# Performance work log

Hardware: AMD Instinct MI355X
Metric: run time of the kernel (lower is better)

The kernel has to match this reference:

```python
import jax, jax.numpy as jnp
import numpy as np

B, N1, N2, E = 128, 128, 384, 1024
N = N1 + N2
D_IN, D_FC = 64, 128
NUM_HEADS = 8.0  # args.num_att_heads
THETA = 1.0      # args.al_scale


def setup_inputs() -> dict:
    key = jax.random.key(0)
    ks = jax.random.split(key, 14)
    c_hs = jax.random.normal(ks[0], (B, N, D_IN), jnp.float32)
    attention = jax.random.uniform(ks[1], (B, N1, N2), jnp.float32)
    coords = jax.random.normal(ks[2], (B, N, 3), jnp.float32)
    upd_coords = coords + 0.1 * jax.random.normal(ks[3], (B, N, 3), jnp.float32)
    c_valid = jnp.ones((B, N), jnp.float32)
    nm = (jax.random.uniform(ks[4], (B, N1)) < 0.7).astype(jnp.float32)
    mapping = (jax.random.uniform(ks[5], (B, N, N)) < 0.05).astype(jnp.float32)
    samelb = jnp.maximum(mapping, (jax.random.uniform(ks[6], (B, N, N)) < 0.1).astype(jnp.float32))
    edge_index = jax.random.randint(ks[7], (B, E, 2), 0, N1, jnp.int32)
    W0 = jax.random.normal(ks[8], (D_IN, D_FC), jnp.float32) * 0.05
    b0 = jnp.zeros((D_FC,), jnp.float32)
    W1 = jax.random.normal(ks[9], (D_FC, D_FC), jnp.float32) * 0.05
    b1 = jnp.zeros((D_FC,), jnp.float32)
    W2 = jax.random.normal(ks[10], (D_FC, D_FC), jnp.float32) * 0.05
    b2 = jnp.zeros((D_FC,), jnp.float32)
    W3 = jax.random.normal(ks[11], (D_FC, 1), jnp.float32) * 0.05
    b3 = jnp.zeros((1,), jnp.float32)
    return dict(c_hs=c_hs, attention=attention, coords=coords, upd_coords=upd_coords,
                c_valid=c_valid, nm=nm, mapping=mapping, samelb=samelb,
                edge_index=edge_index, W0=W0, b0=b0, W1=W1, b1=b1, W2=W2, b2=b2, W3=W3, b3=b3)


def _kabsch(P, Q, m):
    # P, Q: [N1, 3], m: [N1] 0/1 non-modified mask
    Pm = P.mean(0)
    Qm = Q.mean(0)
    h = (P - Pm).T @ (Q - Qm) / NUM_HEADS  # [3,3]
    u, s, vt = jnp.linalg.svd(h)
    d = jnp.sign(jnp.linalg.det(h))
    corr = jnp.diag(jnp.concatenate([jnp.ones((2,), h.dtype), d[None].astype(h.dtype)]))
    r = u @ corr @ vt
    trans = Qm - r @ Pm
    Pp = P @ r.T + trans
    mk = (m > 0.5).astype(P.dtype)[:, None]
    cnt = jnp.maximum(mk.sum() * 3.0, 1.0)
    new_rmsd = (mk * (Pp - Q) ** 2).sum() / cnt        # mse over selected rows
    cen = ((Pp.mean(0) - Qm) ** 2).mean()              # centroid mse
    return new_rmsd, cen


def reference(c_hs, attention, coords, upd_coords, c_valid, nm, mapping, samelb,
              edge_index, W0, b0, W1, b1, W2, b2, W3, b3):
    # --- segment-sum pooling (sum_var_parts) + divide by n1, then FC head ---
    pooled = (c_hs * c_valid[..., None]).sum(axis=1) / float(N1)   # [B, D_IN]
    h = jax.nn.relu(pooled @ W0 + b0)
    h = jax.nn.relu(h @ W1 + b1)
    h = jax.nn.relu(h @ W2 + b2)
    scores = jax.nn.sigmoid(h @ W3 + b3).reshape(-1)               # [B]

    # --- cal_atten_batch + F.normalize(dim=1) ---
    atten = jnp.zeros((B, N, N), c_hs.dtype)
    atten = atten.at[:, :N1, N1:].set(attention)
    atten = atten.at[:, N1:, :N1].set(jnp.swapaxes(attention, 1, 2))
    nrm = jnp.sqrt((atten ** 2).sum(axis=1, keepdims=True))
    atten = atten / jnp.maximum(nrm, 1e-12)

    # --- cal_attn_loss ---
    top = jnp.where(mapping == 1.0, jnp.exp(-(atten * mapping)), 0.0).sum(axis=(1, 2))
    topabot = jnp.where(samelb == 1.0, jnp.exp(-(atten * samelb)), 0.0).sum(axis=(1, 2))
    attn_loss = (top / (topabot - top + 1.0)).sum() * THETA / float(B)

    # --- cal_rmsd_loss: straight-through one-hot mapping + Kabsch/SVD ---
    PP = upd_coords[:, :N1]   # subgraph updated coords
    QQ = coords[:, N1:]       # target graph original coords
    oh = jax.nn.one_hot(jnp.argmax(attention, axis=-1), N2, dtype=attention.dtype)
    st = oh + attention - jax.lax.stop_gradient(attention)         # straight-through
    Qsel = jnp.einsum('bij,bjd->bid', st, QQ)                      # [B, N1, 3]
    new_rmsd, cen = jax.vmap(_kabsch)(PP, Qsel, nm)
    rmsd_loss = new_rmsd.mean()
    centroid_loss = cen.mean()

    # --- cal_pairdst_loss over subgraph edges ---
    sub_c = coords[:, :N1]
    sub_u = upd_coords[:, :N1]
    bidx = jnp.arange(B)[:, None]
    d0 = jnp.sqrt(((sub_c[bidx, edge_index[..., 0]] - sub_c[bidx, edge_index[..., 1]]) ** 2).sum(-1) + 1e-12)
    d1 = jnp.sqrt(((sub_u[bidx, edge_index[..., 0]] - sub_u[bidx, edge_index[..., 1]]) ** 2).sum(-1) + 1e-12)
    pairdst_loss = jnp.abs((d1 - d0).sum(axis=-1)).mean()

    return scores, attn_loss, rmsd_loss, pairdst_loss, centroid_loss
```

## Files before the change

### kernel.cpp

```cpp
#include <hip/hip_runtime.h>
#include <math.h>

#define B_   128
#define N1_  128
#define N2_  384
#define N_   512
#define E_   1024
#define DIN  64
#define DFC  128

#define ACC_TOP  0
#define ACC_BOT  128
#define POOL_OFF 256
#define RNI_OFF  (POOL_OFF + B_*DIN)
#define BI_OFF   (RNI_OFF + B_*N1_)
#define CNI_OFF  (BI_OFF + B_*N1_)

typedef float f4v __attribute__((ext_vector_type(4)));
__device__ __forceinline__ float4 ntl4(const float4* p) {
    f4v v = __builtin_nontemporal_load((const f4v*)p);
    float4 r; r.x = v.x; r.y = v.y; r.z = v.z; r.w = v.w;
    return r;
}

__global__ void k_init(float* ws, float* out) {
    int idx = blockIdx.x * 256 + threadIdx.x;
    if (idx < 256 + B_ * DIN) ws[idx] = 0.f;
    if (idx < B_ * N2_) ws[CNI_OFF + idx] = 0.f;
    if (idx < 4) out[128 + idx] = 0.f;
}

__global__ void k_front(const float* __restrict__ c_hs, const float* __restrict__ c_valid,
                        const float* __restrict__ att, float* __restrict__ ws) {
    __shared__ float4 sred4[256];
    int b = blockIdx.x, y = blockIdx.y, t = threadIdx.x;
    if (y < 8) {
        int chunk = y * 64;
        int d4 = t & 15, rl = t >> 4;
        const float4* X4 = (const float4*)(c_hs + (size_t)b * N_ * DIN);
        const float* V = c_valid + (size_t)b * N_;
        float4 acc = {0.f, 0.f, 0.f, 0.f};
        #pragma unroll
        for (int r = chunk + rl; r < chunk + 64; r += 16) {
            float4 x = ntl4(&X4[r * 16 + d4]);
            float v = V[r];
            acc.x += x.x * v; acc.y += x.y * v; acc.z += x.z * v; acc.w += x.w * v;
        }
        sred4[t] = acc; __syncthreads();
        for (int off = 128; off >= 16; off >>= 1) {
            if (t < off) {
                float4 o = sred4[t + off];
                sred4[t].x += o.x; sred4[t].y += o.y; sred4[t].z += o.z; sred4[t].w += o.w;
            }
            __syncthreads();
        }
        if (t < 16) {
            float4 s = sred4[t];
            float* p = ws + POOL_OFF + b * DIN + t * 4;
            atomicAdd(&p[0], s.x); atomicAdd(&p[1], s.y);
            atomicAdd(&p[2], s.z); atomicAdd(&p[3], s.w);
        }
        return;
    }
    float* colacc = (float*)sred4;
    for (int c = t; c < N2_; c += 256) colacc[c] = 0.f;
    __syncthreads();
    int wv = t >> 6, ln = t & 63;
    int r = (y - 8) * 4 + wv;
    const float* row = att + ((size_t)b * N1_ + r) * N2_;
    float vv[6];
    float ssq = 0.f, best = -1e30f; int bidx = 0;
    #pragma unroll
    for (int q = 0; q < 6; ++q) {
        float v = row[ln + 64 * q];
        vv[q] = v;
        ssq += v * v;
        if (v > best) { best = v; bidx = ln + 64 * q; }
    }
    #pragma unroll
    for (int q = 0; q < 6; ++q) atomicAdd(&colacc[ln + 64 * q], vv[q] * vv[q]);
    for (int off = 32; off > 0; off >>= 1) {
        ssq += __shfl_xor(ssq, off, 64);
        float ov = __shfl_xor(best, off, 64);
        int oi = __shfl_xor(bidx, off, 64);
        if (ov > best || (ov == best && oi < bidx)) { best = ov; bidx = oi; }
    }
    if (ln == 0) {
        ws[RNI_OFF + b * N1_ + r] = 1.f / fmaxf(sqrtf(ssq), 1e-12f);
        ((int*)ws)[BI_OFF + b * N1_ + r] = bidx;
    }
    __syncthreads();
    for (int c = t; c < N2_; c += 256)
        atomicAdd(&ws[CNI_OFF + b * N2_ + c], colacc[c]);
}

__global__ void k_fin(float* __restrict__ ws) {
    int b = blockIdx.x, t = threadIdx.x;
    float v = ws[CNI_OFF + b * N2_ + t];
    ws[CNI_OFF + b * N2_ + t] = 1.f / fmaxf(sqrtf(v), 1e-12f);
}

#define EWS 132
__global__ __launch_bounds__(256, 4)
void k_scan(const float* __restrict__ att, const float* __restrict__ mapping,
            const float* __restrict__ samelb, float* __restrict__ ws) {
    __shared__ float ew[8 * EWS];
    __shared__ float rt[4], rb[4];
    int d = blockIdx.x;
    int xcd = d & 7, kk = d >> 3;
    int b = xcd * 16 + (kk >> 6);
    int tile = kk & 63;
    int t = threadIdx.x;
    float top = 0.f, bot = 0.f;
    int r = t >> 5, c4 = t & 31;
    if (tile < 16) {
        int i0 = tile * 8;
        const float4* m4 = (const float4*)(mapping + ((size_t)b * N_ + i0) * N_);
        const float4* s4 = (const float4*)(samelb + ((size_t)b * N_ + i0) * N_);
        const float4* a4 = (const float4*)(att + ((size_t)b * N1_ + i0) * N2_);
        const float4* cn4 = (const float4*)(ws + CNI_OFF + (size_t)b * N2_);
        float4 md = ntl4(&m4[r * 128 + c4]);
        float4 sd = ntl4(&s4[r * 128 + c4]);
        float4 av[3], mv[3], sv[3], cn[3];
        #pragma unroll
        for (int k = 0; k < 3; ++k) {
            int c = c4 + 32 * k;
            av[k] = a4[r * 96 + c];
            mv[k] = ntl4(&m4[r * 128 + 32 + c]);
            sv[k] = ntl4(&s4[r * 128 + 32 + c]);
            cn[k] = cn4[c];
        }
        top = md.x + md.y + md.z + md.w;
        bot = sd.x + sd.y + sd.z + sd.w;
        #pragma unroll
        for (int k = 0; k < 3; ++k) {
            float e0 = __expf(-av[k].x * cn[k].x);
            float e1 = __expf(-av[k].y * cn[k].y);
            float e2 = __expf(-av[k].z * cn[k].z);
            float e3 = __expf(-av[k].w * cn[k].w);
            top += mv[k].x * e0 + mv[k].y * e1 + mv[k].z * e2 + mv[k].w * e3;
            bot += sv[k].x * e0 + sv[k].y * e1 + sv[k].z * e2 + sv[k].w * e3;
        }
    } else {
        int tb = tile - 16;
        int cr0 = tb * 8;
        const float4* a4 = (const float4*)(att + (size_t)b * N1_ * N2_);
        {
            int j = t >> 1, q = t & 1;
            float4 a = a4[j * 96 + tb * 2 + q];
            float rv = ws[RNI_OFF + b * N1_ + j];
            ew[(4 * q + 0) * EWS + j] = __expf(-a.x * rv);
            ew[(4 * q + 1) * EWS + j] = __expf(-a.y * rv);
            ew[(4 * q + 2) * EWS + j] = __expf(-a.z * rv);
            ew[(4 * q + 3) * EWS + j] = __expf(-a.w * rv);
        }
        const float4* m4 = (const float4*)(mapping + ((size_t)b * N_ + N1_ + cr0) * N_);
        const float4* s4 = (const float4*)(samelb + ((size_t)b * N_ + N1_ + cr0) * N_);
        float4 mL = ntl4(&m4[r * 128 + c4]);
        float4 sL = ntl4(&s4[r * 128 + c4]);
        float4 mR[3], sR[3];
        #pragma unroll
        for (int k = 0; k < 3; ++k) {
            int c = c4 + 32 * k;
            mR[k] = ntl4(&m4[r * 128 + 32 + c]);
            sR[k] = ntl4(&s4[r * 128 + 32 + c]);
        }
        __syncthreads();
        float4 w = *(const float4*)&ew[r * EWS + c4 * 4];
        top = mL.x * w.x + mL.y * w.y + mL.z * w.z + mL.w * w.w;
        bot = sL.x * w.x + sL.y * w.y + sL.z * w.z + sL.w * w.w;
        #pragma unroll
        for (int k = 0; k < 3; ++k) {
            top += mR[k].x + mR[k].y + mR[k].z + mR[k].w;
            bot += sR[k].x + sR[k].y + sR[k].z + sR[k].w;
        }
    }
    for (int off = 32; off > 0; off >>= 1) {
        top += __shfl_down(top, off, 64);
        bot += __shfl_down(bot, off, 64);
    }
    int wv = t >> 6, ln = t & 63;
    if (ln == 0) { rt[wv] = top; rb[wv] = bot; }
    __syncthreads();
    if (t == 0) {
        atomicAdd(&ws[ACC_TOP + b], rt[0] + rt[1] + rt[2] + rt[3]);
        atomicAdd(&ws[ACC_BOT + b], rb[0] + rb[1] + rb[2] + rb[3]);
    }
}

__device__ inline float bred(float* s2, float v, int t) {
    for (int off = 32; off > 0; off >>= 1) v += __shfl_down(v, off, 64);
    if ((t & 63) == 0) s2[t >> 6] = v;
    __syncthreads();
    float r = s2[0] + s2[1];
    __syncthreads();
    return r;
}

__global__ void k_back(const float* __restrict__ coords, const float* __restrict__ upd,
                       const float* __restrict__ nm, const int* __restrict__ ei,
                       const float* __restrict__ W0, const float* __restrict__ b0,
                       const float* __restrict__ W1, const float* __restrict__ b1,
                       const float* __restrict__ W2, const float* __restrict__ b2,
                       const float* __restrict__ W3, const float* __restrict__ b3,
                       const float* __restrict__ ws, float* __restrict__ out) {
    __shared__ float sh[2 * DFC];
    int b = blockIdx.x, t = threadIdx.x;
    if (blockIdx.y == 1) {
        float* pool = sh;
        float* h    = sh + 64;
        __shared__ float part[DFC];
        if (t < DIN) pool[t] = ws[POOL_OFF + b * DIN + t] * (1.0f / 128.0f);
        __syncthreads();
        float a = b0[t];
        #pragma unroll
        for (int i = 0; i < DIN; ++i) a += pool[i] * W0[i * DFC + t];
        float hv = fmaxf(a, 0.f);
        __syncthreads(); h[t] = hv; __syncthreads();
        a = b1[t];
        #pragma unroll
        for (int i = 0; i < DFC; ++i) a += h[i] * W1[i * DFC + t];
        hv = fmaxf(a, 0.f);
        __syncthreads(); h[t] = hv; __syncthreads();
        a = b2[t];
        #pragma unroll
        for (int i = 0; i < DFC; ++i) a += h[i] * W2[i * DFC + t];
        part[t] = fmaxf(a, 0.f) * W3[t];
        __syncthreads();
        for (int off = 64; off > 0; off >>= 1) { if (t < off) part[t] += part[t + off]; __syncthreads(); }
        if (t == 0) out[b] = 1.f / (1.f + expf(-(part[0] + b3[0])));
        return;
    }
    float* s2 = sh;
    __shared__ float Rsh[9], Tsh[3];
    int bidx = ((const int*)ws)[BI_OFF + b * N1_ + t];
    float P[3], Q[3];
    const float* up = upd + ((size_t)b * N_ + t) * 3;
    P[0] = up[0]; P[1] = up[1]; P[2] = up[2];
    const float* qp = coords + ((size_t)b * N_ + N1_ + bidx) * 3;
    Q[0] = qp[0]; Q[1] = qp[1]; Q[2] = qp[2];
    float Pm[3], Qm[3];
    for (int a = 0; a < 3; ++a) Pm[a] = bred(s2, P[a], t) * (1.f / 128.f);
    for (int a = 0; a < 3; ++a) Qm[a] = bred(s2, Q[a], t) * (1.f / 128.f);
    float H[9];
    for (int a = 0; a < 3; ++a)
        for (int c = 0; c < 3; ++c)
            H[a * 3 + c] = bred(s2, (P[a] - Pm[a]) * (Q[c] - Qm[c]), t) * (1.f / 8.f);
    if (t == 0) {
        double Hd[3][3];
        for (int a = 0; a < 3; ++a) for (int c = 0; c < 3; ++c) Hd[a][c] = (double)H[a * 3 + c];
        double A[3][3], V[3][3] = {{1,0,0},{0,1,0},{0,0,1}};
        for (int i = 0; i < 3; ++i)
            for (int j = 0; j < 3; ++j) {
                double z = 0; for (int c = 0; c < 3; ++c) z += Hd[c][i] * Hd[c][j];
                A[i][j] = z;
            }
        for (int sweep = 0; sweep < 8; ++sweep) {
            const int PQ[3][2] = {{0,1},{0,2},{1,2}};
            for (int r = 0; r < 3; ++r) {
                int p = PQ[r][0], q = PQ[r][1];
                double apq = A[p][q];
                if (fabs(apq) < 1e-300) continue;
                double tau = (A[q][q] - A[p][p]) / (2.0 * apq);
                double tt = (tau >= 0 ? 1.0 : -1.0) / (fabs(tau) + sqrt(1.0 + tau * tau));
                double c = 1.0 / sqrt(1.0 + tt * tt), s = tt * c;
                for (int k = 0; k < 3; ++k) { double akp = A[k][p], akq = A[k][q]; A[k][p] = c * akp - s * akq; A[k][q] = s * akp + c * akq; }
                for (int k = 0; k < 3; ++k) { double apk = A[p][k], aqk = A[q][k]; A[p][k] = c * apk - s * aqk; A[q][k] = s * apk + c * aqk; }
                for (int k = 0; k < 3; ++k) { double vkp = V[k][p], vkq = V[k][q]; V[k][p] = c * vkp - s * vkq; V[k][q] = s * vkp + c * vkq; }
            }
        }
        double lam[3] = {A[0][0], A[1][1], A[2][2]};
        int id[3] = {0, 1, 2};
        if (lam[id[0]] < lam[id[1]]) { int x = id[0]; id[0] = id[1]; id[1] = x; }
        if (lam[id[0]] < lam[id[2]]) { int x = id[0]; id[0] = id[2]; id[2] = x; }
        if (lam[id[1]] < lam[id[2]]) { int x = id[1]; id[1] = id[2]; id[2] = x; }
        double u[3][3], v[3][3], sv[3];
        for (int i = 0; i < 3; ++i) {
            for (int k = 0; k < 3; ++k) v[i][k] = V[k][id[i]];
            double uv[3];
            for (int c = 0; c < 3; ++c) uv[c] = Hd[c][0] * v[i][0] + Hd[c][1] * v[i][1] + Hd[c][2] * v[i][2];
            double n = sqrt(uv[0] * uv[0] + uv[1] * uv[1] + uv[2] * uv[2]);
            sv[i] = n;
            if (n > 1e-150) { u[i][0] = uv[0] / n; u[i][1] = uv[1] / n; u[i][2] = uv[2] / n; }
            else { u[i][0] = u[i][1] = u[i][2] = 0.0; }
        }
        if (sv[2] < 1e-12 * fmax(sv[0], 1e-300)) {
            u[2][0] = u[0][1] * u[1][2] - u[0][2] * u[1][1];
            u[2][1] = u[0][2] * u[1][0] - u[0][0] * u[1][2];
            u[2][2] = u[0][0] * u[1][1] - u[0][1] * u[1][0];
        }
        double det = Hd[0][0] * (Hd[1][1] * Hd[2][2] - Hd[1][2] * Hd[2][1])
                   - Hd[0][1] * (Hd[1][0] * Hd[2][2] - Hd[1][2] * Hd[2][0])
                   + Hd[0][2] * (Hd[1][0] * Hd[2][1] - Hd[1][1] * Hd[2][0]);
        double dsg = (det > 0.0) ? 1.0 : ((det < 0.0) ? -1.0 : 0.0);
        for (int a = 0; a < 3; ++a)
            for (int c = 0; c < 3; ++c)
                Rsh[a * 3 + c] = (float)(u[0][a] * v[0][c] + u[1][a] * v[1][c] + dsg * u[2][a] * v[2][c]);
        for (int a = 0; a < 3; ++a)
            Tsh[a] = Qm[a] - (Rsh[a * 3] * Pm[0] + Rsh[a * 3 + 1] * Pm[1] + Rsh[a * 3 + 2] * Pm[2]);
    }
    __syncthreads();
    float Pp[3];
    for (int a = 0; a < 3; ++a)
        Pp[a] = Rsh[a * 3] * P[0] + Rsh[a * 3 + 1] * P[1] + Rsh[a * 3 + 2] * P[2] + Tsh[a];
    float mk = (nm[b * N1_ + t] > 0.5f) ? 1.f : 0.f;
    float dx = Pp[0] - Q[0], dy = Pp[1] - Q[1], dz = Pp[2] - Q[2];
    float rsum = bred(s2, mk * (dx * dx + dy * dy + dz * dz), t);
    float msum = bred(s2, mk, t);
    float Ppm[3];
    for (int a = 0; a < 3; ++a) Ppm[a] = bred(s2, Pp[a], t) * (1.f / 128.f);
    if (t == 0) {
        float cnt = fmaxf(msum * 3.f, 1.f);
        atomicAdd(&out[129], (rsum / cnt) * (1.f / 128.f));
        float cen = 0.f;
        for (int a = 0; a < 3; ++a) { float d2 = Ppm[a] - Qm[a]; cen += d2 * d2; }
        atomicAdd(&out[131], (cen / 3.f) * (1.f / 128.f));
    }
    const float* C = coords + (size_t)b * N_ * 3;
    const float* U = upd + (size_t)b * N_ * 3;
    const int* e = ei + (size_t)b * E_ * 2;
    float acc = 0.f;
    for (int idx = t; idx < E_; idx += 128) {
        int a0 = e[idx * 2], a1 = e[idx * 2 + 1];
        float ex = C[a0 * 3] - C[a1 * 3], ey = C[a0 * 3 + 1] - C[a1 * 3 + 1], ez = C[a0 * 3 + 2] - C[a1 * 3 + 2];
        float d0 = sqrtf(ex * ex + ey * ey + ez * ez + 1e-12f);
        ex = U[a0 * 3] - U[a1 * 3]; ey = U[a0 * 3 + 1] - U[a1 * 3 + 1]; ez = U[a0 * 3 + 2] - U[a1 * 3 + 2];
        float d1 = sqrtf(ex * ex + ey * ey + ez * ez + 1e-12f);
        acc += d1 - d0;
    }
    float psum = bred(s2, acc, t);
    if (t == 0) atomicAdd(&out[130], fabsf(psum) * (1.f / 128.f));
    if (b == 0) {
        float top = ws[ACC_TOP + t], bot = ws[ACC_BOT + t];
        float v = top / (bot - top + 1.0f);
        float s = bred(s2, v, t);
        if (t == 0) out[128] = s * (1.0f / 128.0f);
    }
}

extern "C" void kernel_launch(void* const* d_in, const int* in_sizes, int n_in,
                              void* d_out, int out_size, void* d_ws, size_t ws_size,
                              hipStream_t stream) {
    const float* c_hs      = (const float*)d_in[0];
    const float* attention = (const float*)d_in[1];
    const float* coords    = (const float*)d_in[2];
    const float* upd       = (const float*)d_in[3];
    const float* c_valid   = (const float*)d_in[4];
    const float* nm        = (const float*)d_in[5];
    const float* mapping   = (const float*)d_in[6];
    const float* samelb    = (const float*)d_in[7];
    const int*   ei        = (const int*)d_in[8];
    const float* W0 = (const float*)d_in[9],  *b0 = (const float*)d_in[10];
    const float* W1 = (const float*)d_in[11], *b1 = (const float*)d_in[12];
    const float* W2 = (const float*)d_in[13], *b2 = (const float*)d_in[14];
    const float* W3 = (const float*)d_in[15], *b3 = (const float*)d_in[16];
    float* out = (float*)d_out;
    float* ws  = (float*)d_ws;

    hipLaunchKernelGGL(k_init,  dim3(192),     dim3(256), 0, stream, ws, out);
    hipLaunchKernelGGL(k_front, dim3(B_, 40),  dim3(256), 0, stream, c_hs, c_valid, attention, ws);
    hipLaunchKernelGGL(k_fin,   dim3(B_),      dim3(N2_), 0, stream, ws);
    hipLaunchKernelGGL(k_scan,  dim3(8192),    dim3(256), 0, stream, attention, mapping, samelb, ws);
    hipLaunchKernelGGL(k_back,  dim3(B_, 2),   dim3(128), 0, stream, coords, upd, nm, ei,
                       W0, b0, W1, b1, W2, b2, W3, b3, ws, out);
}
```

Measured before the change: 364.2 us.

## Merge init, front and finalize kernels into one atomic-free preprocessing kernel

Replaces k_init, k_front and k_fin with a single k_pre kernel. Each batch gets one block for pooling and one block for the attention row norms, argmax and column norms, so workspace zeroing and global atomics are no longer needed. The column-norm inverse square root is computed in the same kernel, which removes two launches. It also remaps the batch index in k_scan across XCDs. The trade-off is far fewer blocks in the front stage (256 instead of 5120), each doing a longer serial loop, which may leave the GPU underused.

```diff
diff --git a/kernel.cpp b/kernel.cpp
--- a/kernel.cpp
+++ b/kernel.cpp
@@ -23,25 +23,20 @@
     return r;
 }
 
-__global__ void k_init(float* ws, float* out) {
-    int idx = blockIdx.x * 256 + threadIdx.x;
-    if (idx < 256 + B_ * DIN) ws[idx] = 0.f;
-    if (idx < B_ * N2_) ws[CNI_OFF + idx] = 0.f;
-    if (idx < 4) out[128 + idx] = 0.f;
-}
-
-__global__ void k_front(const float* __restrict__ c_hs, const float* __restrict__ c_valid,
-                        const float* __restrict__ att, float* __restrict__ ws) {
+__global__ void k_pre(const float* __restrict__ c_hs, const float* __restrict__ c_valid,
+                      const float* __restrict__ att, float* __restrict__ ws,
+                      float* __restrict__ out) {
     __shared__ float4 sred4[256];
-    int b = blockIdx.x, y = blockIdx.y, t = threadIdx.x;
-    if (y < 8) {
-        int chunk = y * 64;
+    __shared__ float colp[8][N2_];
+    int b = blockIdx.x, t = threadIdx.x;
+    if (blockIdx.y == 0) {
+        if (t == 0) { ws[ACC_TOP + b] = 0.f; ws[ACC_BOT + b] = 0.f; }
+        if (b == 0 && t < 4) out[128 + t] = 0.f;
         int d4 = t & 15, rl = t >> 4;
         const float4* X4 = (const float4*)(c_hs + (size_t)b * N_ * DIN);
         const float* V = c_valid + (size_t)b * N_;
         float4 acc = {0.f, 0.f, 0.f, 0.f};
-        #pragma unroll
-        for (int r = chunk + rl; r < chunk + 64; r += 16) {
+        for (int r = rl; r < N_; r += 16) {
             float4 x = ntl4(&X4[r * 16 + d4]);
             float v = V[r];
             acc.x += x.x * v; acc.y += x.y * v; acc.z += x.z * v; acc.w += x.w * v;
@@ -57,47 +52,53 @@
         if (t < 16) {
             float4 s = sred4[t];
             float* p = ws + POOL_OFF + b * DIN + t * 4;
-            atomicAdd(&p[0], s.x); atomicAdd(&p[1], s.y);
-            atomicAdd(&p[2], s.z); atomicAdd(&p[3], s.w);
+            p[0] = s.x; p[1] = s.y; p[2] = s.z; p[3] = s.w;
         }
         return;
     }
-    float* colacc = (float*)sred4;
-    for (int c = t; c < N2_; c += 256) colacc[c] = 0.f;
-    __syncthreads();
-    int wv = t >> 6, ln = t & 63;
-    int r = (y - 8) * 4 + wv;
-    const float* row = att + ((size_t)b * N1_ + r) * N2_;
-    float vv[6];
-    float ssq = 0.f, best = -1e30f; int bidx = 0;
+    int lane = t & 31, grp = t >> 5;
+    const float4* a4 = (const float4*)(att + (size_t)b * N1_ * N2_);
+    float4 cs[3] = {{0,0,0,0},{0,0,0,0},{0,0,0,0}};
+    for (int rr = 0; rr < N1_; rr += 8) {
+        int r = rr + grp;
+        float ssq = 0.f, best = -1e30f; int bidx = 0;
+        #pragma unroll
+        for (int c = 0; c < 3; ++c) {
+            float4 v = a4[(size_t)r * 96 + c * 32 + lane];
+            cs[c].x += v.x * v.x; cs[c].y += v.y * v.y;
+            cs[c].z += v.z * v.z; cs[c].w += v.w * v.w;
+            ssq += v.x * v.x + v.y * v.y + v.z * v.z + v.w * v.w;
+            int cb = (c * 32 + lane) * 4;
+            if (v.x > best) { best = v.x; bidx = cb; }
+            if (v.y > best) { best = v.y; bidx = cb + 1; }
+            if (v.z > best) { best = v.z; bidx = cb + 2; }
+            if (v.w > best) { best = v.w; bidx = cb + 3; }
+        }
+        for (int off = 16; off > 0; off >>= 1) {
+            ssq += __shfl_xor(ssq, off, 64);
+            float ov = __shfl_xor(best, off, 64);
+            int oi = __shfl_xor(bidx, off, 64);
+            if (ov > best || (ov == best && oi < bidx)) { best = ov; bidx = oi; }
+        }
+        if (lane == 0) {
+            ws[RNI_OFF + b * N1_ + r] = 1.f / fmaxf(sqrtf(ssq), 1e-12f);
+            ((int*)ws)[BI_OFF + b * N1_ + r] = bidx;
+        }
+    }
     #pragma unroll
-    for (int q = 0; q < 6; ++q) {
-        float v = row[ln + 64 * q];
-        vv[q] = v;
-        ssq += v * v;
-        if (v > best) { best = v; bidx = ln + 64 * q; }
-    }
-    #pragma unroll
-    for (int q = 0; q < 6; ++q) atomicAdd(&colacc[ln + 64 * q], vv[q] * vv[q]);
-    for (int off = 32; off > 0; off >>= 1) {
-        ssq += __shfl_xor(ssq, off, 64);
-        float ov = __shfl_xor(best, off, 64);
-        int oi = __shfl_xor(bidx, off, 64);
-        if (ov > best || (ov == best && oi < bidx)) { best = ov; bidx = oi; }
-    }
-    if (ln == 0) {
-        ws[RNI_OFF + b * N1_ + r] = 1.f / fmaxf(sqrtf(ssq), 1e-12f);
-        ((int*)ws)[BI_OFF + b * N1_ + r] = bidx;
-    }
-    __syncthreads();
-    for (int c = t; c < N2_; c += 256)
-        atomicAdd(&ws[CNI_OFF + b * N2_ + c], colacc[c]);
-}
-
-__global__ void k_fin(float* __restrict__ ws) {
-    int b = blockIdx.x, t = threadIdx.x;
-    float v = ws[CNI_OFF + b * N2_ + t];
-    ws[CNI_OFF + b * N2_ + t] = 1.f / fmaxf(sqrtf(v), 1e-12f);
+    for (int c = 0; c < 3; ++c) {
+        int fc = (c * 32 + lane) * 4;
+        colp[grp][fc]     = cs[c].x;
+        colp[grp][fc + 1] = cs[c].y;
+        colp[grp][fc + 2] = cs[c].z;
+        colp[grp][fc + 3] = cs[c].w;
+    }
+    __syncthreads();
+    for (int cc = t; cc < N2_; cc += 256) {
+        float s = colp[0][cc] + colp[1][cc] + colp[2][cc] + colp[3][cc]
+                + colp[4][cc] + colp[5][cc] + colp[6][cc] + colp[7][cc];
+        ws[CNI_OFF + b * N2_ + cc] = 1.f / fmaxf(sqrtf(s), 1e-12f);
+    }
 }
 
 #define EWS 132
@@ -108,7 +109,7 @@
     __shared__ float rt[4], rb[4];
     int d = blockIdx.x;
     int xcd = d & 7, kk = d >> 3;
-    int b = xcd * 16 + (kk >> 6);
+    int b = xcd + 8 * (kk >> 6);
     int tile = kk & 63;
     int t = threadIdx.x;
     float top = 0.f, bot = 0.f;
@@ -357,10 +358,8 @@
     float* out = (float*)d_out;
     float* ws  = (float*)d_ws;
 
-    hipLaunchKernelGGL(k_init,  dim3(192),     dim3(256), 0, stream, ws, out);
-    hipLaunchKernelGGL(k_front, dim3(B_, 40),  dim3(256), 0, stream, c_hs, c_valid, attention, ws);
-    hipLaunchKernelGGL(k_fin,   dim3(B_),      dim3(N2_), 0, stream, ws);
-    hipLaunchKernelGGL(k_scan,  dim3(8192),    dim3(256), 0, stream, attention, mapping, samelb, ws);
-    hipLaunchKernelGGL(k_back,  dim3(B_, 2),   dim3(128), 0, stream, coords, upd, nm, ei,
+    hipLaunchKernelGGL(k_pre,  dim3(B_, 2), dim3(256), 0, stream, c_hs, c_valid, attention, ws, out);
+    hipLaunchKernelGGL(k_scan, dim3(8192),  dim3(256), 0, stream, attention, mapping, samelb, ws);
+    hipLaunchKernelGGL(k_back, dim3(B_, 2), dim3(128), 0, stream, coords, upd, nm, ei,
                        W0, b0, W1, b1, W2, b2, W3, b3, ws, out);
 }
```

Result: no change. 359.3 us (-1.4%).
